# Kernel optimization log

Measured on AMD Instinct MI355X. Metric: run time of the kernel, lower is better.

## Reference

```python
import jax, jax.numpy as jnp
import numpy as np

N_EMBD = 1024
N_HEAD = 16


def setup_inputs() -> dict:
    key = jax.random.key(0)
    k1, k2, k3 = jax.random.split(key, 3)
    B, T, C = 4, 2048, N_EMBD
    x = jax.random.normal(k1, (B, T, C), dtype=jnp.float32)
    # params (bias=False)
    w_attn = jax.random.normal(k2, (C, 3 * C), dtype=jnp.float32) * (C ** -0.5)
    w_proj = jax.random.normal(k3, (C, C), dtype=jnp.float32) * (C ** -0.5)
    return {"x": x, "w_attn": w_attn, "w_proj": w_proj}


def reference(x, w_attn, w_proj):
    B, T, C = x.shape
    H = N_HEAD
    hs = C // H
    qkv = x @ w_attn  # [B,T,3C]
    q, k, v = jnp.split(qkv, 3, axis=-1)
    # [B,H,T,hs]
    q = q.reshape(B, T, H, hs).transpose(0, 2, 1, 3)
    k = k.reshape(B, T, H, hs).transpose(0, 2, 1, 3)
    v = v.reshape(B, T, H, hs).transpose(0, 2, 1, 3)
    wei = jnp.einsum('bhqd,bhkd->bhqk', q, k) * (hs ** -0.5)
    causal = jnp.tril(jnp.ones((T, T), dtype=bool))
    wei = jnp.where(causal[None, None], wei, -jnp.inf)
    wei = jax.nn.softmax(wei, axis=-1)
    # dropout p=0.0 -> identity
    y = jnp.einsum('bhqk,bhkd->bhqd', wei, v)
    y = y.transpose(0, 2, 1, 3).reshape(B, T, C)
    return y @ w_proj
```

## Files before the change

kernel.cpp:

```cpp
#include <hip/hip_runtime.h>
#include <math.h>
#include <stdint.h>

#define B_BATCH 4
#define T_SEQ   2048
#define C_EMB   1024
#define NH      16
#define HS      64

typedef _Float16 half_t;
typedef __attribute__((ext_vector_type(8))) _Float16 half8;
typedef __attribute__((ext_vector_type(4))) _Float16 half4;
typedef __attribute__((ext_vector_type(2))) __fp16 pk16x2;
typedef __attribute__((ext_vector_type(4))) float f32x4;

static __device__ __forceinline__ f32x4 mfma_k16(half4 a, half4 b, f32x4 c) {
#if __has_builtin(__builtin_amdgcn_mfma_f32_16x16x16f16)
    return __builtin_amdgcn_mfma_f32_16x16x16f16(a, b, c, 0, 0, 0);
#else
    half8 a8 = {a.x, a.y, a.z, a.w, (_Float16)0, (_Float16)0, (_Float16)0, (_Float16)0};
    half8 b8 = {b.x, b.y, b.z, b.w, (_Float16)0, (_Float16)0, (_Float16)0, (_Float16)0};
    return __builtin_amdgcn_mfma_f32_16x16x32_f16(a8, b8, c, 0, 0, 0);
#endif
}

static __device__ __forceinline__ void stage16(const void* g, void* lds_base) {
#if __has_builtin(__builtin_amdgcn_global_load_lds)
    __builtin_amdgcn_global_load_lds(
        (const __attribute__((address_space(1))) void*)g,
        (__attribute__((address_space(3))) void*)lds_base, 16, 0, 0);
#else
    const int lane = threadIdx.x & 63;
    ((uint4*)lds_base)[lane] = *(const uint4*)g;
#endif
}

__global__ __launch_bounds__(256) void prep_kernel(const float* __restrict__ x,
                                                   half_t* __restrict__ xh,
                                                   const float* __restrict__ wa,
                                                   half_t* __restrict__ waT,
                                                   const float* __restrict__ wp,
                                                   half_t* __restrict__ wpT) {
    const int blk = blockIdx.x;
    const int tid = threadIdx.x;

    if (blk < 4096) {
        const int i = blk * 256 + tid;
        const float4 a = *(const float4*)(x + (size_t)i * 8);
        const float4 b = *(const float4*)(x + (size_t)i * 8 + 4);
        const pk16x2 h0 = __builtin_amdgcn_cvt_pkrtz(a.x, a.y);
        const pk16x2 h1 = __builtin_amdgcn_cvt_pkrtz(a.z, a.w);
        const pk16x2 h2 = __builtin_amdgcn_cvt_pkrtz(b.x, b.y);
        const pk16x2 h3 = __builtin_amdgcn_cvt_pkrtz(b.z, b.w);
        half8 o = {(_Float16)h0.x, (_Float16)h0.y, (_Float16)h1.x, (_Float16)h1.y,
                   (_Float16)h2.x, (_Float16)h2.y, (_Float16)h3.x, (_Float16)h3.y};
        *(half8*)(xh + (size_t)i * 8) = o;
        return;
    }

    const float* W;
    half_t* WT;
    int K, N, bb;
    if (blk < 4096 + 768) {
        bb = blk - 4096; W = wa; WT = waT; K = 1024; N = 3072;
    } else {
        bb = blk - 4864; W = wp; WT = wpT; K = 1024; N = 1024;
    }
    const int ntiles = N / 64;
    const int n0 = (bb % ntiles) * 64;
    const int k0 = (bb / ntiles) * 64;

    __shared__ float t[64][65];
    const int r = tid >> 4, c4 = (tid & 15) * 4;
#pragma unroll
    for (int p = 0; p < 4; ++p) {
        const float4 g = *(const float4*)(W + (size_t)(k0 + p * 16 + r) * N + n0 + c4);
        t[p * 16 + r][c4 + 0] = g.x;
        t[p * 16 + r][c4 + 1] = g.y;
        t[p * 16 + r][c4 + 2] = g.z;
        t[p * 16 + r][c4 + 3] = g.w;
    }
    __syncthreads();
#pragma unroll
    for (int p = 0; p < 4; ++p) {
        const int n = p * 16 + r;
        half4 s = {(_Float16)t[c4 + 0][n], (_Float16)t[c4 + 1][n],
                   (_Float16)t[c4 + 2][n], (_Float16)t[c4 + 3][n]};
        *(half4*)(WT + (size_t)(n0 + n) * K + k0 + c4) = s;
    }
}

#define BK2 64

__global__ __launch_bounds__(512, 2) void gemm256(const half_t* __restrict__ A,
                                                  const half_t* __restrict__ Bt,
                                                  half_t* __restrict__ Cout,
                                                  int M, int N, int K) {
    __shared__ __align__(16) half_t SM[65536];

    const int tid  = threadIdx.x;
    const int lane = tid & 63;
    const int wid  = tid >> 6;
    const int l16  = lane & 15;
    const int quad = lane >> 4;

    const int nwg = gridDim.x;
    const int cpx = nwg >> 3;
    const int bid = (blockIdx.x & 7) * cpx + (blockIdx.x >> 3);
    const int nbx = N >> 8;
    const int bx = bid % nbx;
    const int by = bid / nbx;
    const size_t m0 = (size_t)by << 8;
    const size_t n0 = (size_t)bx << 8;

    const int warpM = (wid >> 2) * 128;
    const int wn    = (wid & 3) * 64;
    const int NTk   = K >> 6;

    const int srow = tid >> 3;
    const int scsw = (tid & 7) ^ (srow & 7);
    const half_t* gAs = A  + (m0 + srow) * (size_t)K + scsw * 8;
    const half_t* gBs = Bt + (n0 + srow) * (size_t)K + scsw * 8;

    f32x4 acc[8][4];
#pragma unroll
    for (int i = 0; i < 8; ++i)
#pragma unroll
        for (int j = 0; j < 4; ++j) acc[i][j] = (f32x4){0.f, 0.f, 0.f, 0.f};

    auto ldA = [&](const half_t* Ab, int mt, int kk) -> half8 {
        const int r = warpM + mt * 16 + l16;
        const int c = (kk * 4 + quad) ^ (l16 & 7);
        return *(const half8*)(Ab + r * 64 + c * 8);
    };
    auto ldB = [&](const half_t* Bb, int nt, int kk) -> half8 {
        const int r = wn + nt * 16 + l16;
        const int c = (kk * 4 + quad) ^ (l16 & 7);
        return *(const half8*)(Bb + r * 64 + c * 8);
    };

#pragma unroll
    for (int s = 0; s < 4; ++s)
        stage16(gAs + (size_t)(s * 64) * K, SM + s * 4096 + wid * 512);
#pragma unroll
    for (int s = 0; s < 4; ++s)
        stage16(gBs + (size_t)(s * 64) * K, SM + 16384 + s * 4096 + wid * 512);
    if (NTk > 1) {
#pragma unroll
        for (int s = 0; s < 4; ++s)
            stage16(gBs + (size_t)(s * 64) * K + BK2, SM + 49152 + s * 4096 + wid * 512);
        asm volatile("s_waitcnt vmcnt(4)" ::: "memory");
    } else {
        asm volatile("s_waitcnt vmcnt(0)" ::: "memory");
    }
    __builtin_amdgcn_s_barrier();
    __builtin_amdgcn_sched_barrier(0);

    auto tile_body = [&](int t, half_t* Ac, half_t* Bc, half_t* An) {
        const int kA = (t + 1) * BK2;
        const int kB = (t + 2) * BK2;
        const bool doA = (t + 1) < NTk;
        const bool doB = (t + 2) < NTk;

        half8 fb[4][2];

        if (doA) {
            stage16(gAs + (size_t)(0 * 64) * K + kA, An + 0 * 4096 + wid * 512);
            stage16(gAs + (size_t)(1 * 64) * K + kA, An + 1 * 4096 + wid * 512);
        }
#pragma unroll
        for (int nt = 0; nt < 4; ++nt) {
            fb[nt][0] = ldB(Bc, nt, 0);
            fb[nt][1] = ldB(Bc, nt, 1);
        }
        {
            half8 a00 = ldA(Ac, 0, 0), a01 = ldA(Ac, 0, 1);
            half8 a10 = ldA(Ac, 1, 0), a11 = ldA(Ac, 1, 1);
            __builtin_amdgcn_s_barrier();
            __builtin_amdgcn_s_setprio(1);
#pragma unroll
            for (int nt = 0; nt < 4; ++nt) {
                acc[0][nt] = __builtin_amdgcn_mfma_f32_16x16x32_f16(a00, fb[nt][0], acc[0][nt], 0, 0, 0);
                acc[0][nt] = __builtin_amdgcn_mfma_f32_16x16x32_f16(a01, fb[nt][1], acc[0][nt], 0, 0, 0);
                acc[1][nt] = __builtin_amdgcn_mfma_f32_16x16x32_f16(a10, fb[nt][0], acc[1][nt], 0, 0, 0);
                acc[1][nt] = __builtin_amdgcn_mfma_f32_16x16x32_f16(a11, fb[nt][1], acc[1][nt], 0, 0, 0);
            }
            __builtin_amdgcn_s_setprio(0);
        }
        if (doA) {
            stage16(gAs + (size_t)(2 * 64) * K + kA, An + 2 * 4096 + wid * 512);
            stage16(gAs + (size_t)(3 * 64) * K + kA, An + 3 * 4096 + wid * 512);
        }
        {
            half8 a00 = ldA(Ac, 2, 0), a01 = ldA(Ac, 2, 1);
            half8 a10 = ldA(Ac, 3, 0), a11 = ldA(Ac, 3, 1);
            __builtin_amdgcn_s_barrier();
            __builtin_amdgcn_s_setprio(1);
#pragma unroll
            for (int nt = 0; nt < 4; ++nt) {
                acc[2][nt] = __builtin_amdgcn_mfma_f32_16x16x32_f16(a00, fb[nt][0], acc[2][nt], 0, 0, 0);
                acc[2][nt] = __builtin_amdgcn_mfma_f32_16x16x32_f16(a01, fb[nt][1], acc[2][nt], 0, 0, 0);
                acc[3][nt] = __builtin_amdgcn_mfma_f32_16x16x32_f16(a10, fb[nt][0], acc[3][nt], 0, 0, 0);
                acc[3][nt] = __builtin_amdgcn_mfma_f32_16x16x32_f16(a11, fb[nt][1], acc[3][nt], 0, 0, 0);
            }
            __builtin_amdgcn_s_setprio(0);
        }
        if (doB) {
            stage16(gBs + (size_t)(0 * 64) * K + kB, Bc + 0 * 4096 + wid * 512);
            stage16(gBs + (size_t)(1 * 64) * K + kB, Bc + 1 * 4096 + wid * 512);
        }
        {
            half8 a00 = ldA(Ac, 4, 0), a01 = ldA(Ac, 4, 1);
            half8 a10 = ldA(Ac, 5, 0), a11 = ldA(Ac, 5, 1);
            __builtin_amdgcn_s_barrier();
            __builtin_amdgcn_s_setprio(1);
#pragma unroll
            for (int nt = 0; nt < 4; ++nt) {
                acc[4][nt] = __builtin_amdgcn_mfma_f32_16x16x32_f16(a00, fb[nt][0], acc[4][nt], 0, 0, 0);
                acc[4][nt] = __builtin_amdgcn_mfma_f32_16x16x32_f16(a01, fb[nt][1], acc[4][nt], 0, 0, 0);
                acc[5][nt] = __builtin_amdgcn_mfma_f32_16x16x32_f16(a10, fb[nt][0], acc[5][nt], 0, 0, 0);
                acc[5][nt] = __builtin_amdgcn_mfma_f32_16x16x32_f16(a11, fb[nt][1], acc[5][nt], 0, 0, 0);
            }
            __builtin_amdgcn_s_setprio(0);
        }
        if (doB) {
            stage16(gBs + (size_t)(2 * 64) * K + kB, Bc + 2 * 4096 + wid * 512);
            stage16(gBs + (size_t)(3 * 64) * K + kB, Bc + 3 * 4096 + wid * 512);
        }
        {
            half8 a00 = ldA(Ac, 6, 0), a01 = ldA(Ac, 6, 1);
            half8 a10 = ldA(Ac, 7, 0), a11 = ldA(Ac, 7, 1);
            __builtin_amdgcn_s_barrier();
            __builtin_amdgcn_s_setprio(1);
#pragma unroll
            for (int nt = 0; nt < 4; ++nt) {
                acc[6][nt] = __builtin_amdgcn_mfma_f32_16x16x32_f16(a00, fb[nt][0], acc[6][nt], 0, 0, 0);
                acc[6][nt] = __builtin_amdgcn_mfma_f32_16x16x32_f16(a01, fb[nt][1], acc[6][nt], 0, 0, 0);
                acc[7][nt] = __builtin_amdgcn_mfma_f32_16x16x32_f16(a10, fb[nt][0], acc[7][nt], 0, 0, 0);
                acc[7][nt] = __builtin_amdgcn_mfma_f32_16x16x32_f16(a11, fb[nt][1], acc[7][nt], 0, 0, 0);
            }
            __builtin_amdgcn_s_setprio(0);
        }
        if (doB) {
            asm volatile("s_waitcnt vmcnt(4)" ::: "memory");
        } else if (doA) {
            asm volatile("s_waitcnt vmcnt(0)" ::: "memory");
        }
        __builtin_amdgcn_s_barrier();
        __builtin_amdgcn_sched_barrier(0);
    };

    for (int tt = 0; tt < NTk; tt += 2) {
        tile_body(tt, SM, SM + 16384, SM + 32768);
        if (tt + 1 < NTk)
            tile_body(tt + 1, SM + 32768, SM + 49152, SM);
    }

    __syncthreads();
    float* cw = (float*)SM + wid * 1024;
    const int rrow = lane >> 2;
    const int cseg = (lane & 3) * 16;
#pragma unroll
    for (int mt = 0; mt < 8; ++mt) {
#pragma unroll
        for (int nt = 0; nt < 4; ++nt)
            *(f32x4*)&cw[(nt * 16 + l16) * 16 + quad * 4] = acc[mt][nt];
        half_t tmp[16];
#pragma unroll
        for (int jj = 0; jj < 16; ++jj)
            tmp[jj] = (half_t)cw[(cseg + jj) * 16 + rrow];
        half_t* dst = Cout + (m0 + warpM + mt * 16 + rrow) * (size_t)N + n0 + wn + cseg;
        *(half8*)(dst)     = *(const half8*)(tmp);
        *(half8*)(dst + 8) = *(const half8*)(tmp + 8);
    }
}

__global__ __launch_bounds__(256) void gemm_bt_a64(const half_t* __restrict__ A,
                                                   const half_t* __restrict__ Bt,
                                                   float* __restrict__ Cout,
                                                   int M, int N, int K) {
    __shared__ half_t As[64 * 32];
    __shared__ half_t Bs[128 * 32];

    const int tid  = threadIdx.x;
    const int lane = tid & 63;
    const int wid  = tid >> 6;
    const int l16  = lane & 15;
    const int quad = lane >> 4;

    const int m0 = blockIdx.y * 64;
    const int n0 = blockIdx.x * 128;
    const int wm = (wid & 1) * 32;
    const int wn = (wid >> 1) * 64;

    const half_t* gA  = A  + (size_t)(m0 + wid * 16      + (lane >> 2)) * K + (lane & 3) * 8;
    const half_t* gB0 = Bt + (size_t)(n0 + wid * 16      + (lane >> 2)) * K + (lane & 3) * 8;
    const half_t* gB1 = Bt + (size_t)(n0 + wid * 16 + 64 + (lane >> 2)) * K + (lane & 3) * 8;

    half_t* lA  = As + (size_t)wid * 512;
    half_t* lB0 = Bs + (size_t)wid * 512;
    half_t* lB1 = Bs + (size_t)(wid + 4) * 512;

    f32x4 acc[2][4];
#pragma unroll
    for (int i = 0; i < 2; ++i)
#pragma unroll
        for (int j = 0; j < 4; ++j) acc[i][j] = (f32x4){0.f, 0.f, 0.f, 0.f};

    for (int k0 = 0; k0 < K; k0 += 32) {
        __syncthreads();
        stage16(gA + k0, lA);
        stage16(gB0 + k0, lB0);
        stage16(gB1 + k0, lB1);
        __syncthreads();

        half8 fa[2], fb[4];
#pragma unroll
        for (int mt = 0; mt < 2; ++mt)
            fa[mt] = *(const half8*)(As + (wm + mt * 16 + l16) * 32 + quad * 8);
#pragma unroll
        for (int nt = 0; nt < 4; ++nt)
            fb[nt] = *(const half8*)(Bs + (wn + nt * 16 + l16) * 32 + quad * 8);
#pragma unroll
        for (int mt = 0; mt < 2; ++mt)
#pragma unroll
            for (int nt = 0; nt < 4; ++nt)
                acc[mt][nt] = __builtin_amdgcn_mfma_f32_16x16x32_f16(
                    fa[mt], fb[nt], acc[mt][nt], 0, 0, 0);
    }

#pragma unroll
    for (int mt = 0; mt < 2; ++mt)
#pragma unroll
        for (int nt = 0; nt < 4; ++nt)
#pragma unroll
            for (int r = 0; r < 4; ++r) {
                const size_t row = m0 + wm + mt * 16 + quad * 4 + r;
                const size_t col = n0 + wn + nt * 16 + l16;
                Cout[row * N + col] = acc[mt][nt][r];
            }
}

#define KL_STRIDE 72
#define VT_STRIDE 72
#define SCALE_EXP2 0.18033688f

__global__ __launch_bounds__(256, 4) void attn_mfma(const half_t* __restrict__ qkv,
                                                    half_t* __restrict__ y) {
    __shared__ half_t Kl[64 * KL_STRIDE];
    __shared__ half_t Vt[64 * VT_STRIDE];
    __shared__ float Lstat[64];

    const int tid  = threadIdx.x;
    const int wid  = tid >> 6;
    const int lane = tid & 63;
    const int l16  = lane & 15;
    const int quad = lane >> 4;

    const int L = blockIdx.x;
    const int g = L & 63;
    const int s = L >> 6;
    const int h = g & 15;
    const int b = g >> 4;

    const size_t rs = 3 * C_EMB;
    const half_t* qb = qkv + (size_t)b * T_SEQ * rs + h * HS;
    const half_t* kb = qb + C_EMB;
    const half_t* vb = qb + 2 * C_EMB;

    const int srow = tid >> 2;
    const int scol = (tid & 3) * 16;
    const int rp   = tid & 31;
    const int dblk = tid >> 5;

    const int qrel = wid * 16 + l16;

#pragma unroll 1
    for (int j = 0; j < 2; ++j) {
        const int qh = (j == 0) ? (31 - s) : s;
        const int q0 = qh * 64;

        __syncthreads();
        {
            const half_t* src = qb + (size_t)(q0 + srow) * rs + scol;
            half_t* dst = Kl + srow * KL_STRIDE + scol;
            *(half8*)(dst)     = *(const half8*)(src);
            *(half8*)(dst + 8) = *(const half8*)(src + 8);
        }
        __syncthreads();

        half8 aQ[2];
#pragma unroll
        for (int s2 = 0; s2 < 2; ++s2)
            aQ[s2] = *(const half8*)(Kl + (wid * 16 + l16) * KL_STRIDE + s2 * 32 + quad * 8);

        f32x4 O[4];
#pragma unroll
        for (int dt = 0; dt < 4; ++dt) O[dt] = (f32x4){0.f, 0.f, 0.f, 0.f};
        float lw = 0.f;

        for (int kt = 0; kt <= qh; ++kt) {
            const int k0 = kt * 64;
            const bool diag = (kt == qh);
            __syncthreads();

            {
                const half_t* src = kb + (size_t)(k0 + srow) * rs + scol;
                half_t* dst = Kl + srow * KL_STRIDE + scol;
                *(half8*)(dst)     = *(const half8*)(src);
                *(half8*)(dst + 8) = *(const half8*)(src + 8);
            }
            {
                const uint4 va = *(const uint4*)(vb + (size_t)(k0 + 2 * rp) * rs + dblk * 8);
                const uint4 vc = *(const uint4*)(vb + (size_t)(k0 + 2 * rp + 1) * rs + dblk * 8);
                const uint32_t a[4] = {va.x, va.y, va.z, va.w};
                const uint32_t c[4] = {vc.x, vc.y, vc.z, vc.w};
                unsigned short* vts = (unsigned short*)Vt;
#pragma unroll
                for (int u = 0; u < 4; ++u) {
                    const int d0 = dblk * 8 + 2 * u;
                    const uint32_t w0 = (a[u] & 0xffffu) | (c[u] << 16);
                    const uint32_t w1 = (a[u] >> 16) | (c[u] & 0xffff0000u);
                    *(uint32_t*)(vts + (d0 + 0) * VT_STRIDE + 2 * rp) = w0;
                    *(uint32_t*)(vts + (d0 + 1) * VT_STRIDE + 2 * rp) = w1;
                }
            }
            __syncthreads();

#pragma unroll
            for (int mt = 0; mt < 4; ++mt) {
                const half8 aK0 = *(const half8*)(Kl + (mt * 16 + l16) * KL_STRIDE + quad * 8);
                const half8 aK1 = *(const half8*)(Kl + (mt * 16 + l16) * KL_STRIDE + 32 + quad * 8);
                f32x4 sa = (f32x4){0.f, 0.f, 0.f, 0.f};
                sa = __builtin_amdgcn_mfma_f32_16x16x32_f16(aK0, aQ[0], sa, 0, 0, 0);
                sa = __builtin_amdgcn_mfma_f32_16x16x32_f16(aK1, aQ[1], sa, 0, 0, 0);

                const int kbase = mt * 16 + quad * 4;
                float p[4];
#pragma unroll
                for (int r = 0; r < 4; ++r)
                    p[r] = __builtin_amdgcn_exp2f(sa[r] * SCALE_EXP2);
                if (diag) {
#pragma unroll
                    for (int r = 0; r < 4; ++r)
                        if (kbase + r > qrel) p[r] = 0.f;
                }
                lw += (p[0] + p[1]) + (p[2] + p[3]);

                const half4 pa = {(_Float16)p[0], (_Float16)p[1],
                                  (_Float16)p[2], (_Float16)p[3]};
#pragma unroll
                for (int dt = 0; dt < 4; ++dt) {
                    const half4 bV = *(const half4*)(Vt + (dt * 16 + l16) * VT_STRIDE +
                                                     mt * 16 + quad * 4);
                    O[dt] = mfma_k16(pa, bV, O[dt]);
                }
            }
        }

        lw += __shfl_xor(lw, 16);
        lw += __shfl_xor(lw, 32);
        if (quad == 0) Lstat[wid * 16 + l16] = lw;
        __syncthreads();
#pragma unroll
        for (int r = 0; r < 4; ++r) {
            const int rowl = wid * 16 + quad * 4 + r;
            const float inv = 1.f / Lstat[rowl];
#pragma unroll
            for (int dt = 0; dt < 4; ++dt)
                Vt[rowl * VT_STRIDE + dt * 16 + l16] = (half_t)(O[dt][r] * inv);
        }
        __syncthreads();
        {
            half_t* dst = y + ((size_t)b * T_SEQ + q0 + srow) * C_EMB + h * HS + scol;
            const half_t* src = Vt + srow * VT_STRIDE + scol;
            *(half8*)(dst)     = *(const half8*)(src);
            *(half8*)(dst + 8) = *(const half8*)(src + 8);
        }
    }
}

extern "C" void kernel_launch(void* const* d_in, const int* in_sizes, int n_in,
                              void* d_out, int out_size, void* d_ws, size_t ws_size,
                              hipStream_t stream) {
    const float* x      = (const float*)d_in[0];
    const float* w_attn = (const float*)d_in[1];
    const float* w_proj = (const float*)d_in[2];
    float* out = (float*)d_out;

    half_t* xh   = (half_t*)d_ws;
    half_t* waT  = xh   + (size_t)8192 * 1024;
    half_t* wpT  = waT  + (size_t)3072 * 1024;
    half_t* qkvh = wpT  + (size_t)1024 * 1024;
    half_t* yh   = qkvh + (size_t)8192 * 3072;

    prep_kernel<<<5120, 256, 0, stream>>>(x, xh, w_attn, waT, w_proj, wpT);

    gemm256<<<dim3(384), 512, 0, stream>>>(xh, waT, qkvh, 8192, 3072, 1024);

    attn_mfma<<<dim3(1024), 256, 0, stream>>>(qkvh, yh);

    gemm_bt_a64<<<dim3(8, 128), 256, 0, stream>>>(yh, wpT, out, 8192, 1024, 1024);
}
```

Before: 268.1 us.

## Prefetch next K/V tile into registers and XOR-swizzle attention LDS layout

The attention kernel now loads the next K and V tile from global memory into registers while the current tile is being computed, so global latency overlaps with the MFMA work. The padded LDS strides (72) are replaced by an unpadded 64-wide layout with an XOR swizzle on 16-byte chunks to avoid bank conflicts. This lowers LDS use and hides load latency, at the cost of more live registers under a launch bound of 4 blocks per SM and more complex address arithmetic.

```diff
diff --git a/kernel.cpp b/kernel.cpp
--- a/kernel.cpp
+++ b/kernel.cpp
@@ -341,14 +341,12 @@
             }
 }
 
-#define KL_STRIDE 72
-#define VT_STRIDE 72
 #define SCALE_EXP2 0.18033688f
 
 __global__ __launch_bounds__(256, 4) void attn_mfma(const half_t* __restrict__ qkv,
                                                     half_t* __restrict__ y) {
-    __shared__ half_t Kl[64 * KL_STRIDE];
-    __shared__ half_t Vt[64 * VT_STRIDE];
+    __shared__ __align__(16) half_t Kl[64 * 64];
+    __shared__ __align__(16) half_t Vt[64 * 64];
     __shared__ float Lstat[64];
 
     const int tid  = threadIdx.x;
@@ -370,10 +368,18 @@
 
     const int srow = tid >> 2;
     const int scol = (tid & 3) * 16;
+    const int sc2  = (tid & 3) * 2;
     const int rp   = tid & 31;
     const int dblk = tid >> 5;
 
     const int qrel = wid * 16 + l16;
+
+    auto kswz = [&](int row, int chunk) -> half_t* {
+        return Kl + row * 64 + ((chunk ^ (row & 7)) << 3);
+    };
+    auto vswz = [&](int row, int chunk) -> half_t* {
+        return Vt + row * 64 + ((chunk ^ (row & 7)) << 3);
+    };
 
 #pragma unroll 1
     for (int j = 0; j < 2; ++j) {
@@ -383,16 +389,26 @@
         __syncthreads();
         {
             const half_t* src = qb + (size_t)(q0 + srow) * rs + scol;
-            half_t* dst = Kl + srow * KL_STRIDE + scol;
-            *(half8*)(dst)     = *(const half8*)(src);
-            *(half8*)(dst + 8) = *(const half8*)(src + 8);
+            const half8 q0r = *(const half8*)(src);
+            const half8 q1r = *(const half8*)(src + 8);
+            *(half8*)kswz(srow, sc2)     = q0r;
+            *(half8*)kswz(srow, sc2 + 1) = q1r;
+        }
+        half8 kp0, kp1;
+        uint4 vpa, vpc;
+        {
+            const half_t* ksrc = kb + (size_t)srow * rs + scol;
+            kp0 = *(const half8*)(ksrc);
+            kp1 = *(const half8*)(ksrc + 8);
+            const half_t* vsrc = vb + (size_t)(2 * rp) * rs + dblk * 8;
+            vpa = *(const uint4*)(vsrc);
+            vpc = *(const uint4*)(vsrc + rs);
         }
         __syncthreads();
 
         half8 aQ[2];
-#pragma unroll
-        for (int s2 = 0; s2 < 2; ++s2)
-            aQ[s2] = *(const half8*)(Kl + (wid * 16 + l16) * KL_STRIDE + s2 * 32 + quad * 8);
+        aQ[0] = *(const half8*)kswz(wid * 16 + l16, quad);
+        aQ[1] = *(const half8*)kswz(wid * 16 + l16, 4 + quad);
 
         f32x4 O[4];
 #pragma unroll
@@ -400,37 +416,39 @@
         float lw = 0.f;
 
         for (int kt = 0; kt <= qh; ++kt) {
-            const int k0 = kt * 64;
             const bool diag = (kt == qh);
             __syncthreads();
 
+            *(half8*)kswz(srow, sc2)     = kp0;
+            *(half8*)kswz(srow, sc2 + 1) = kp1;
             {
-                const half_t* src = kb + (size_t)(k0 + srow) * rs + scol;
-                half_t* dst = Kl + srow * KL_STRIDE + scol;
-                *(half8*)(dst)     = *(const half8*)(src);
-                *(half8*)(dst + 8) = *(const half8*)(src + 8);
-            }
-            {
-                const uint4 va = *(const uint4*)(vb + (size_t)(k0 + 2 * rp) * rs + dblk * 8);
-                const uint4 vc = *(const uint4*)(vb + (size_t)(k0 + 2 * rp + 1) * rs + dblk * 8);
-                const uint32_t a[4] = {va.x, va.y, va.z, va.w};
-                const uint32_t c[4] = {vc.x, vc.y, vc.z, vc.w};
-                unsigned short* vts = (unsigned short*)Vt;
+                const uint32_t a0[4] = {vpa.x, vpa.y, vpa.z, vpa.w};
+                const uint32_t c0[4] = {vpc.x, vpc.y, vpc.z, vpc.w};
 #pragma unroll
                 for (int u = 0; u < 4; ++u) {
                     const int d0 = dblk * 8 + 2 * u;
-                    const uint32_t w0 = (a[u] & 0xffffu) | (c[u] << 16);
-                    const uint32_t w1 = (a[u] >> 16) | (c[u] & 0xffff0000u);
-                    *(uint32_t*)(vts + (d0 + 0) * VT_STRIDE + 2 * rp) = w0;
-                    *(uint32_t*)(vts + (d0 + 1) * VT_STRIDE + 2 * rp) = w1;
+                    const uint32_t w0 = (a0[u] & 0xffffu) | (c0[u] << 16);
+                    const uint32_t w1 = (a0[u] >> 16) | (c0[u] & 0xffff0000u);
+                    *(uint32_t*)((unsigned short*)vswz(d0,     rp >> 2) + (rp & 3) * 2) = w0;
+                    *(uint32_t*)((unsigned short*)vswz(d0 + 1, rp >> 2) + (rp & 3) * 2) = w1;
                 }
             }
             __syncthreads();
 
+            if (kt < qh) {
+                const int kn = (kt + 1) * 64;
+                const half_t* ksrc = kb + (size_t)(kn + srow) * rs + scol;
+                kp0 = *(const half8*)(ksrc);
+                kp1 = *(const half8*)(ksrc + 8);
+                const half_t* vsrc = vb + (size_t)(kn + 2 * rp) * rs + dblk * 8;
+                vpa = *(const uint4*)(vsrc);
+                vpc = *(const uint4*)(vsrc + rs);
+            }
+
 #pragma unroll
             for (int mt = 0; mt < 4; ++mt) {
-                const half8 aK0 = *(const half8*)(Kl + (mt * 16 + l16) * KL_STRIDE + quad * 8);
-                const half8 aK1 = *(const half8*)(Kl + (mt * 16 + l16) * KL_STRIDE + 32 + quad * 8);
+                const half8 aK0 = *(const half8*)kswz(mt * 16 + l16, quad);
+                const half8 aK1 = *(const half8*)kswz(mt * 16 + l16, 4 + quad);
                 f32x4 sa = (f32x4){0.f, 0.f, 0.f, 0.f};
                 sa = __builtin_amdgcn_mfma_f32_16x16x32_f16(aK0, aQ[0], sa, 0, 0, 0);
                 sa = __builtin_amdgcn_mfma_f32_16x16x32_f16(aK1, aQ[1], sa, 0, 0, 0);
@@ -451,8 +469,9 @@
                                   (_Float16)p[2], (_Float16)p[3]};
 #pragma unroll
                 for (int dt = 0; dt < 4; ++dt) {
-                    const half4 bV = *(const half4*)(Vt + (dt * 16 + l16) * VT_STRIDE +
-                                                     mt * 16 + quad * 4);
+                    const half_t* pv = vswz(dt * 16 + l16, 2 * mt + (quad >> 1)) +
+                                       (quad & 1) * 4;
+                    const half4 bV = *(const half4*)pv;
                     O[dt] = mfma_k16(pa, bV, O[dt]);
                 }
             }
@@ -468,14 +487,14 @@
             const float inv = 1.f / Lstat[rowl];
 #pragma unroll
             for (int dt = 0; dt < 4; ++dt)
-                Vt[rowl * VT_STRIDE + dt * 16 + l16] = (half_t)(O[dt][r] * inv);
+                *(vswz(rowl, 2 * dt + (l16 >> 3)) + (l16 & 7)) =
+                    (half_t)(O[dt][r] * inv);
         }
         __syncthreads();
         {
             half_t* dst = y + ((size_t)b * T_SEQ + q0 + srow) * C_EMB + h * HS + scol;
-            const half_t* src = Vt + srow * VT_STRIDE + scol;
-            *(half8*)(dst)     = *(const half8*)(src);
-            *(half8*)(dst + 8) = *(const half8*)(src + 8);
+            *(half8*)(dst)     = *(const half8*)vswz(srow, sc2);
+            *(half8*)(dst + 8) = *(const half8*)vswz(srow, sc2 + 1);
         }
     }
 }
```

Result: faster. 261.5 us (-2.5%).
